# Optimization experiments

Hardware: AMD Instinct MI355X
Metric: run time of the kernel (lower is better)

Reference implementation:

```python
import jax, jax.numpy as jnp
import numpy as np

N_NODES = 100000
N_EDGES = 3200000
BATCH = 16
HIDDEN = 64


def setup_inputs() -> dict:
    key = jax.random.key(0)
    k_mu, k_ei, k_w1, k_b1, k_w2, k_b2 = jax.random.split(key, 6)
    mu = jax.random.normal(k_mu, (BATCH, N_NODES), dtype=jnp.float32)
    edge_index = jax.random.randint(k_ei, (2, N_EDGES), 0, N_NODES, dtype=jnp.int64)
    # MLP params: Linear(1, hidden) -> GELU -> Linear(hidden, 1)
    W1 = jax.random.normal(k_w1, (1, HIDDEN), dtype=jnp.float32) * (1.0 / np.sqrt(1))
    b1 = jax.random.normal(k_b1, (HIDDEN,), dtype=jnp.float32) * 0.02
    W2 = jax.random.normal(k_w2, (HIDDEN, 1), dtype=jnp.float32) * (1.0 / np.sqrt(HIDDEN))
    b2 = jax.random.normal(k_b2, (1,), dtype=jnp.float32) * 0.02
    return {"mu": mu, "edge_index": edge_index, "W1": W1, "b1": b1, "W2": W2, "b2": b2}


def reference(mu, edge_index, W1, b1, W2, b2):
    row, col = edge_index[0], edge_index[1]
    B, N = mu.shape
    # degree of each destination node (clamped at 1)
    deg = jax.ops.segment_sum(jnp.ones_like(row, dtype=mu.dtype), row, num_segments=N)
    deg = jnp.maximum(deg, 1.0)  # [N]
    # batched message aggregation: gather source values, scatter-add to rows
    msgs = mu[:, col].T                                    # [E, B]
    agg = jax.ops.segment_sum(msgs, row, num_segments=N)   # [N, B]
    out = agg.T / deg[None, :]                             # [B, N]
    # tiny MLP applied per scalar: 1 -> hidden -> 1 with exact (erf) GELU
    h = jax.nn.gelu(out[..., None] * W1[0][None, None, :] + b1, approximate=False)  # [B, N, H]
    y = jnp.einsum('bnh,h->bn', h, W2[:, 0]) + b2[0]       # [B, N]
    return y
```

## Files before the change

### kernel.cpp

```cpp
#include <hip/hip_runtime.h>
#include <hip/hip_fp16.h>

#define N_NODES 100000
#define N_EDGES 3200000
#define BATCH   16
#define HIDDEN  64

#define NBINS   512
#define NPB     196
#define NSH     8
#define CAP_SH  1024
#define CAP_BIN 8192
#define EPB     8192
#define MAXW    16

#define PBLKS   391
#define TBLKS   196
#define LBLKS   17

#define LUT_SIZE  8192
#define LUT_LO    (-16.0f)
#define LUT_SCALE (LUT_SIZE / 32.0f)

typedef int v4i __attribute__((ext_vector_type(4)));

__global__ __launch_bounds__(512) void fused_part_prep_kernel(
    const int* __restrict__ ei, unsigned int* __restrict__ gcnt,
    unsigned int* __restrict__ packed,
    const float* __restrict__ mu, __half* __restrict__ mu_h,
    const float* __restrict__ W1, const float* __restrict__ b1,
    const float* __restrict__ W2, const float* __restrict__ b2,
    float* __restrict__ lut) {
  __shared__ int aux[NBINS];
  __shared__ int dlt[NBINS];
  __shared__ int wsum[8];
  __shared__ unsigned int stag[EPB];
  __shared__ unsigned short sbin[EPB];

  int blk = blockIdx.x;
  int t = threadIdx.x;

  if (blk < TBLKS + LBLKS) {
    if (blk < TBLKS) {
      int n = blk * 512 + t;
      if (n >= N_NODES) return;
      float4 o[4];
#pragma unroll
      for (int q = 0; q < 4; ++q) {
        o[q].x = mu[(q * 4 + 0) * N_NODES + n];
        o[q].y = mu[(q * 4 + 1) * N_NODES + n];
        o[q].z = mu[(q * 4 + 2) * N_NODES + n];
        o[q].w = mu[(q * 4 + 3) * N_NODES + n];
      }
      __half2 hh[8];
#pragma unroll
      for (int q = 0; q < 4; ++q) {
        hh[2 * q]     = __floats2half2_rn(o[q].x, o[q].y);
        hh[2 * q + 1] = __floats2half2_rn(o[q].z, o[q].w);
      }
      int4 w0 = make_int4(*(int*)&hh[0], *(int*)&hh[1], *(int*)&hh[2], *(int*)&hh[3]);
      int4 w1 = make_int4(*(int*)&hh[4], *(int*)&hh[5], *(int*)&hh[6], *(int*)&hh[7]);
      int4* dst = (int4*)(mu_h + (size_t)n * BATCH);
      dst[0] = w0;
      dst[1] = w1;
    } else {
      int i = (blk - TBLKS) * 512 + t;
      if (i > LUT_SIZE) return;
      float x = LUT_LO + (float)i / LUT_SCALE;
      float acc = b2[0];
      for (int h = 0; h < HIDDEN; ++h) {
        float z = fmaf(x, W1[h], b1[h]);
        float g = 0.5f * z * (1.0f + erff(z * 0.70710678118654752f));
        acc = fmaf(g, W2[h], acc);
      }
      lut[i] = acc;
    }
    return;
  }

  int pblk = blk - (TBLKS + LBLKS);
  int base = pblk * EPB;
  int nvalid = min(EPB, N_EDGES - base);
  int sh = pblk & (NSH - 1);
  aux[t] = 0;
  __syncthreads();

  unsigned int pk[16];
  int bn[16];
  int rk[16];
  if (t * 16 + 16 <= nvalid) {
    const v4i* rp = (const v4i*)(ei + base + t * 16);
    const v4i* cp = (const v4i*)(ei + N_EDGES + base + t * 16);
    v4i rr[4], cc[4];
#pragma unroll
    for (int q = 0; q < 4; ++q) {
      rr[q] = rp[q];
      cc[q] = cp[q];
    }
#pragma unroll
    for (int q = 0; q < 4; ++q) {
#pragma unroll
      for (int u = 0; u < 4; ++u) {
        int k = q * 4 + u;
        int r = rr[q][u];
        int c = cc[q][u];
        int b = r / NPB;
        int rl = r - b * NPB;
        pk[k] = ((unsigned int)rl << 17) | (unsigned int)c;
        bn[k] = b;
      }
    }
#pragma unroll
    for (int k = 0; k < 16; ++k) rk[k] = atomicAdd(&aux[bn[k]], 1);
  } else {
#pragma unroll
    for (int k = 0; k < 16; ++k) {
      int e = t * 16 + k;
      if (e < nvalid) {
        int r = ei[base + e];
        int c = ei[N_EDGES + base + e];
        int b = r / NPB;
        int rl = r - b * NPB;
        pk[k] = ((unsigned int)rl << 17) | (unsigned int)c;
        bn[k] = b;
        rk[k] = atomicAdd(&aux[b], 1);
      } else {
        bn[k] = -1;
      }
    }
  }
  __syncthreads();

  int lane = t & 63;
  int wid = t >> 6;
  int v = aux[t];

  unsigned int gb = v ? atomicAdd(&gcnt[t * NSH + sh], (unsigned int)v) : 0u;

  int sv = v;
#pragma unroll
  for (int d = 1; d < 64; d <<= 1) {
    int n = __shfl_up(sv, d, 64);
    if (lane >= d) sv += n;
  }
  if (lane == 63) wsum[wid] = sv;
  __syncthreads();
  if (t < 8) {
    int s = wsum[t];
#pragma unroll
    for (int d = 1; d < 8; d <<= 1) {
      int n = __shfl_up(s, d, 8);
      if (t >= d) s += n;
    }
    wsum[t] = s;
  }
  __syncthreads();
  int pexcl = sv + (wid ? wsum[wid - 1] : 0) - v;
  aux[t] = pexcl;
  dlt[t] = (int)(sh * CAP_SH + gb) - pexcl;
  __syncthreads();

#pragma unroll
  for (int k = 0; k < 16; ++k) {
    if (bn[k] >= 0) {
      int p = aux[bn[k]] + rk[k];
      stag[p] = pk[k];
      sbin[p] = (unsigned short)bn[k];
    }
  }
  __syncthreads();

  unsigned int lim = (unsigned int)((sh + 1) * CAP_SH);
  for (int i = t; i < nvalid; i += 512) {
    int b = sbin[i];
    unsigned int pos = (unsigned int)(i + dlt[b]);
    if (pos < lim)
      packed[(size_t)b * CAP_BIN + pos] = stag[i];
  }
}

__global__ __launch_bounds__(512) void scatter_apply_kernel(
    const unsigned int* __restrict__ gcnt, const unsigned int* __restrict__ packed,
    const __half* __restrict__ mu_h, const float* __restrict__ lut,
    float* __restrict__ out) {
  __shared__ unsigned int scol[CAP_BIN];
  __shared__ int dcnt[NPB];
  __shared__ int ebase[NPB];
  __shared__ int wpart[4];
  __shared__ int scnt_s[NSH];

  int t = threadIdx.x;
  int bin = blockIdx.x;

  const unsigned int* pp = packed + (size_t)bin * CAP_BIN;

  if (t < NPB) dcnt[t] = 0;
  if (t < NSH) scnt_s[t] = min((int)gcnt[bin * NSH + t], CAP_SH);
  __syncthreads();

  unsigned int w[MAXW];
  {
    const uint4* pp4 = (const uint4*)pp;
#pragma unroll
    for (int q = 0; q < 4; ++q) {
      uint4 a = pp4[t * 4 + q];
      w[q * 4 + 0] = a.x;
      w[q * 4 + 1] = a.y;
      w[q * 4 + 2] = a.z;
      w[q * 4 + 3] = a.w;
    }
  }

  int rk[MAXW];
#pragma unroll
  for (int k = 0; k < MAXW; ++k) {
    int i = t * 16 + k;
    int off = i & (CAP_SH - 1);
    rk[k] = (off < scnt_s[i >> 10]) ? atomicAdd(&dcnt[w[k] >> 17], 1) : 0;
  }
  __syncthreads();

  int v = 0, sv = 0;
  if (t < 256) {
    v = (t < NPB) ? dcnt[t] : 0;
    int lane = t & 63;
    sv = v;
#pragma unroll
    for (int d = 1; d < 64; d <<= 1) {
      int n = __shfl_up(sv, d, 64);
      if (lane >= d) sv += n;
    }
    if (lane == 63) wpart[t >> 6] = sv;
  }
  __syncthreads();
  if (t < 256) {
    int wid = t >> 6;
    int off = 0;
#pragma unroll
    for (int q = 0; q < 3; ++q)
      if (wid > q) off += wpart[q];
    if (t < NPB) ebase[t] = sv + off - v;
  }
  __syncthreads();

#pragma unroll
  for (int k = 0; k < MAXW; ++k) {
    int i = t * 16 + k;
    int off = i & (CAP_SH - 1);
    if (off < scnt_s[i >> 10]) {
      int rl = (int)(w[k] >> 17);
      scol[ebase[rl] + rk[k]] = w[k] & 0x1FFFFu;
    }
  }
  __syncthreads();

  const __half2* mu2 = (const __half2*)mu_h;
  int j2 = t & 7;
  int nsl = t >> 3;
  int binBase = bin * NPB;

#pragma unroll
  for (int pass = 0; pass < 4; ++pass) {
    int nl = pass * 64 + nsl;
    if (nl < NPB) {
      int node = binBase + nl;
      if (node < N_NODES) {
        int s = ebase[nl];
        int e = s + dcnt[nl];
        float2 a0 = {0.f, 0.f}, a1 = {0.f, 0.f};
        float2 a2 = {0.f, 0.f}, a3 = {0.f, 0.f};
        int i = s;
        for (; i + 8 <= e; i += 8) {
          int c0 = (int)scol[i];
          int c1 = (int)scol[i + 1];
          int c2 = (int)scol[i + 2];
          int c3 = (int)scol[i + 3];
          int c4 = (int)scol[i + 4];
          int c5 = (int)scol[i + 5];
          int c6 = (int)scol[i + 6];
          int c7 = (int)scol[i + 7];
          __half2 v0 = mu2[(size_t)c0 * 8 + j2];
          __half2 v1 = mu2[(size_t)c1 * 8 + j2];
          __half2 v2 = mu2[(size_t)c2 * 8 + j2];
          __half2 v3 = mu2[(size_t)c3 * 8 + j2];
          __half2 v4 = mu2[(size_t)c4 * 8 + j2];
          __half2 v5 = mu2[(size_t)c5 * 8 + j2];
          __half2 v6 = mu2[(size_t)c6 * 8 + j2];
          __half2 v7 = mu2[(size_t)c7 * 8 + j2];
          float2 f0 = __half22float2(v0);
          float2 f1 = __half22float2(v1);
          float2 f2 = __half22float2(v2);
          float2 f3 = __half22float2(v3);
          float2 f4 = __half22float2(v4);
          float2 f5 = __half22float2(v5);
          float2 f6 = __half22float2(v6);
          float2 f7 = __half22float2(v7);
          a0.x += f0.x + f4.x; a0.y += f0.y + f4.y;
          a1.x += f1.x + f5.x; a1.y += f1.y + f5.y;
          a2.x += f2.x + f6.x; a2.y += f2.y + f6.y;
          a3.x += f3.x + f7.x; a3.y += f3.y + f7.y;
        }
        for (; i + 4 <= e; i += 4) {
          int c0 = (int)scol[i];
          int c1 = (int)scol[i + 1];
          int c2 = (int)scol[i + 2];
          int c3 = (int)scol[i + 3];
          __half2 v0 = mu2[(size_t)c0 * 8 + j2];
          __half2 v1 = mu2[(size_t)c1 * 8 + j2];
          __half2 v2 = mu2[(size_t)c2 * 8 + j2];
          __half2 v3 = mu2[(size_t)c3 * 8 + j2];
          float2 f0 = __half22float2(v0);
          float2 f1 = __half22float2(v1);
          float2 f2 = __half22float2(v2);
          float2 f3 = __half22float2(v3);
          a0.x += f0.x; a0.y += f0.y;
          a1.x += f1.x; a1.y += f1.y;
          a2.x += f2.x; a2.y += f2.y;
          a3.x += f3.x; a3.y += f3.y;
        }
        for (; i < e; ++i) {
          float2 f = __half22float2(mu2[(size_t)scol[i] * 8 + j2]);
          a0.x += f.x; a0.y += f.y;
        }
        float sx = (a0.x + a1.x) + (a2.x + a3.x);
        float sy = (a0.y + a1.y) + (a2.y + a3.y);
        float dinv = 1.0f / (float)max(e - s, 1);

        float xs[2] = {sx * dinv, sy * dinv};
#pragma unroll
        for (int q = 0; q < 2; ++q) {
          float u = (xs[q] - LUT_LO) * LUT_SCALE;
          u = fminf(fmaxf(u, 0.0f), (float)LUT_SIZE - 0.001f);
          int ii = (int)u;
          float frac = u - (float)ii;
          float lo = lut[ii];
          float hi = lut[ii + 1];
          __builtin_nontemporal_store(fmaf(hi - lo, frac, lo),
                                      &out[(size_t)(2 * j2 + q) * N_NODES + node]);
        }
      }
    }
  }
}

extern "C" void kernel_launch(void* const* d_in, const int* in_sizes, int n_in,
                              void* d_out, int out_size, void* d_ws, size_t ws_size,
                              hipStream_t stream) {
  const float* mu = (const float*)d_in[0];
  const int*   ei = (const int*)d_in[1];
  const float* W1 = (const float*)d_in[2];
  const float* b1 = (const float*)d_in[3];
  const float* W2 = (const float*)d_in[4];
  const float* b2 = (const float*)d_in[5];
  float* out = (float*)d_out;

  __half* mu_h = (__half*)d_ws;
  float* lut  = (float*)(mu_h + (size_t)N_NODES * BATCH);
  unsigned int* gcnt = (unsigned int*)(lut + LUT_SIZE + 1);
  unsigned int* packed = gcnt + NBINS * NSH;

  (void)hipMemsetAsync(gcnt, 0, NBINS * NSH * sizeof(unsigned int), stream);

  fused_part_prep_kernel<<<PBLKS + TBLKS + LBLKS, 512, 0, stream>>>(
      ei, gcnt, packed, mu, mu_h, W1, b1, W2, b2, lut);

  scatter_apply_kernel<<<NBINS, 512, 0, stream>>>(gcnt, packed, mu_h, lut, out);
}
```

Baseline: 124.4 us.

## Fold transpose and LUT work into partition blocks; stage LUT in shared memory

The half-precision transpose of mu and the GELU-MLP lookup-table build no longer run in their own blocks. Each of the 391 partition blocks now does a slice of both before its bucketing work, so the launch shrinks to the partition grid. The scatter/apply kernel copies the whole 8193-entry LUT into shared memory per block and interpolates from there, and its output stores become ordinary stores instead of nontemporal ones. Both kernels get a min-blocks launch-bounds hint. The trade-off is that every scatter block pays a 32 KB LUT copy and carries more LDS, which can lower occupancy. The partition blocks also have to wait at the barrier for the serial 64-step erf loop.

```diff
diff --git a/kernel.cpp b/kernel.cpp
--- a/kernel.cpp
+++ b/kernel.cpp
@@ -15,8 +15,8 @@
 #define MAXW    16
 
 #define PBLKS   391
-#define TBLKS   196
-#define LBLKS   17
+#define NPT     256
+#define LPT     21
 
 #define LUT_SIZE  8192
 #define LUT_LO    (-16.0f)
@@ -24,7 +24,7 @@
 
 typedef int v4i __attribute__((ext_vector_type(4)));
 
-__global__ __launch_bounds__(512) void fused_part_prep_kernel(
+__global__ __launch_bounds__(512, 4) void fused_part_prep_kernel(
     const int* __restrict__ ei, unsigned int* __restrict__ gcnt,
     unsigned int* __restrict__ packed,
     const float* __restrict__ mu, __half* __restrict__ mu_h,
@@ -37,13 +37,14 @@
   __shared__ unsigned int stag[EPB];
   __shared__ unsigned short sbin[EPB];
 
-  int blk = blockIdx.x;
+  int pblk = blockIdx.x;
   int t = threadIdx.x;
 
-  if (blk < TBLKS + LBLKS) {
-    if (blk < TBLKS) {
-      int n = blk * 512 + t;
-      if (n >= N_NODES) return;
+  aux[t] = 0;
+
+  if (t < NPT) {
+    int n = pblk * NPT + t;
+    if (n < N_NODES) {
       float4 o[4];
 #pragma unroll
       for (int q = 0; q < 4; ++q) {
@@ -63,9 +64,10 @@
       int4* dst = (int4*)(mu_h + (size_t)n * BATCH);
       dst[0] = w0;
       dst[1] = w1;
-    } else {
-      int i = (blk - TBLKS) * 512 + t;
-      if (i > LUT_SIZE) return;
+    }
+  } else if (t < NPT + LPT) {
+    int i = pblk * LPT + (t - NPT);
+    if (i <= LUT_SIZE) {
       float x = LUT_LO + (float)i / LUT_SCALE;
       float acc = b2[0];
       for (int h = 0; h < HIDDEN; ++h) {
@@ -75,15 +77,12 @@
       }
       lut[i] = acc;
     }
-    return;
-  }
-
-  int pblk = blk - (TBLKS + LBLKS);
+  }
+  __syncthreads();
+
   int base = pblk * EPB;
   int nvalid = min(EPB, N_EDGES - base);
   int sh = pblk & (NSH - 1);
-  aux[t] = 0;
-  __syncthreads();
 
   unsigned int pk[16];
   int bn[16];
@@ -179,11 +178,12 @@
   }
 }
 
-__global__ __launch_bounds__(512) void scatter_apply_kernel(
+__global__ __launch_bounds__(512, 4) void scatter_apply_kernel(
     const unsigned int* __restrict__ gcnt, const unsigned int* __restrict__ packed,
     const __half* __restrict__ mu_h, const float* __restrict__ lut,
     float* __restrict__ out) {
   __shared__ unsigned int scol[CAP_BIN];
+  __shared__ float lut_s[LUT_SIZE + 1];
   __shared__ int dcnt[NPB];
   __shared__ int ebase[NPB];
   __shared__ int wpart[4];
@@ -196,6 +196,14 @@
 
   if (t < NPB) dcnt[t] = 0;
   if (t < NSH) scnt_s[t] = min((int)gcnt[bin * NSH + t], CAP_SH);
+
+  {
+    const float4* l4 = (const float4*)lut;
+    float4* s4 = (float4*)lut_s;
+#pragma unroll
+    for (int j = 0; j < 4; ++j) s4[t + j * 512] = l4[t + j * 512];
+    if (t == 0) lut_s[LUT_SIZE] = lut[LUT_SIZE];
+  }
   __syncthreads();
 
   unsigned int w[MAXW];
@@ -333,10 +341,9 @@
           u = fminf(fmaxf(u, 0.0f), (float)LUT_SIZE - 0.001f);
           int ii = (int)u;
           float frac = u - (float)ii;
-          float lo = lut[ii];
-          float hi = lut[ii + 1];
-          __builtin_nontemporal_store(fmaf(hi - lo, frac, lo),
-                                      &out[(size_t)(2 * j2 + q) * N_NODES + node]);
+          float lo = lut_s[ii];
+          float hi = lut_s[ii + 1];
+          out[(size_t)(2 * j2 + q) * N_NODES + node] = fmaf(hi - lo, frac, lo);
         }
       }
     }
@@ -361,7 +368,7 @@
 
   (void)hipMemsetAsync(gcnt, 0, NBINS * NSH * sizeof(unsigned int), stream);
 
-  fused_part_prep_kernel<<<PBLKS + TBLKS + LBLKS, 512, 0, stream>>>(
+  fused_part_prep_kernel<<<PBLKS, 512, 0, stream>>>(
       ei, gcnt, packed, mu, mu_h, W1, b1, W2, b2, lut);
 
   scatter_apply_kernel<<<NBINS, 512, 0, stream>>>(gcnt, packed, mu_h, lut, out);
```

After: 133.0 us. 6.9% more time.

## Replace per-node CSR sort with LDS float atomic accumulation in scatter kernel

Applied to the files above, without the earlier changes.

The scatter kernel no longer builds a per-node CSR inside each bin (atomic rank, prefix scan, reorder). Instead it compacts the edge words into LDS, counts degrees, and then walks edges in order, gathering half-precision mu values and accumulating them into a padded shared-memory accumulator with float atomics. The output stage then reads the accumulator per (batch, node) with coalesced stores. This removes two barriers and the scan, at the cost of many LDS float atomics with possible contention and a non-deterministic summation order.

```diff
diff --git a/kernel.cpp b/kernel.cpp
--- a/kernel.cpp
+++ b/kernel.cpp
@@ -12,7 +12,7 @@
 #define CAP_SH  1024
 #define CAP_BIN 8192
 #define EPB     8192
-#define MAXW    16
+#define ACCW    17
 
 #define PBLKS   391
 #define TBLKS   196
@@ -184,161 +184,77 @@
     const __half* __restrict__ mu_h, const float* __restrict__ lut,
     float* __restrict__ out) {
   __shared__ unsigned int scol[CAP_BIN];
+  __shared__ float acc[NPB * ACCW];
   __shared__ int dcnt[NPB];
-  __shared__ int ebase[NPB];
-  __shared__ int wpart[4];
   __shared__ int scnt_s[NSH];
 
   int t = threadIdx.x;
   int bin = blockIdx.x;
-
   const unsigned int* pp = packed + (size_t)bin * CAP_BIN;
 
+  for (int i = t; i < NPB * ACCW; i += 512) acc[i] = 0.0f;
   if (t < NPB) dcnt[t] = 0;
   if (t < NSH) scnt_s[t] = min((int)gcnt[bin * NSH + t], CAP_SH);
   __syncthreads();
 
-  unsigned int w[MAXW];
+  int pfx[NSH + 1];
+  pfx[0] = 0;
+#pragma unroll
+  for (int q = 0; q < NSH; ++q) pfx[q + 1] = pfx[q] + scnt_s[q];
+  int cnt = pfx[NSH];
+
   {
     const uint4* pp4 = (const uint4*)pp;
+    uint4 a[4];
+#pragma unroll
+    for (int q = 0; q < 4; ++q) a[q] = pp4[t * 4 + q];
 #pragma unroll
     for (int q = 0; q < 4; ++q) {
-      uint4 a = pp4[t * 4 + q];
-      w[q * 4 + 0] = a.x;
-      w[q * 4 + 1] = a.y;
-      w[q * 4 + 2] = a.z;
-      w[q * 4 + 3] = a.w;
-    }
-  }
-
-  int rk[MAXW];
-#pragma unroll
-  for (int k = 0; k < MAXW; ++k) {
-    int i = t * 16 + k;
-    int off = i & (CAP_SH - 1);
-    rk[k] = (off < scnt_s[i >> 10]) ? atomicAdd(&dcnt[w[k] >> 17], 1) : 0;
-  }
-  __syncthreads();
-
-  int v = 0, sv = 0;
-  if (t < 256) {
-    v = (t < NPB) ? dcnt[t] : 0;
-    int lane = t & 63;
-    sv = v;
-#pragma unroll
-    for (int d = 1; d < 64; d <<= 1) {
-      int n = __shfl_up(sv, d, 64);
-      if (lane >= d) sv += n;
-    }
-    if (lane == 63) wpart[t >> 6] = sv;
-  }
-  __syncthreads();
-  if (t < 256) {
-    int wid = t >> 6;
-    int off = 0;
-#pragma unroll
-    for (int q = 0; q < 3; ++q)
-      if (wid > q) off += wpart[q];
-    if (t < NPB) ebase[t] = sv + off - v;
-  }
-  __syncthreads();
-
-#pragma unroll
-  for (int k = 0; k < MAXW; ++k) {
-    int i = t * 16 + k;
-    int off = i & (CAP_SH - 1);
-    if (off < scnt_s[i >> 10]) {
-      int rl = (int)(w[k] >> 17);
-      scol[ebase[rl] + rk[k]] = w[k] & 0x1FFFFu;
-    }
-  }
-  __syncthreads();
-
+      unsigned int wq[4] = {a[q].x, a[q].y, a[q].z, a[q].w};
+#pragma unroll
+      for (int u = 0; u < 4; ++u) {
+        int i = t * 16 + q * 4 + u;
+        int sh = i >> 10;
+        int off = i & (CAP_SH - 1);
+        if (off < scnt_s[sh]) {
+          unsigned int wv = wq[u];
+          scol[pfx[sh] + off] = wv;
+          atomicAdd(&dcnt[wv >> 17], 1);
+        }
+      }
+    }
+  }
+  __syncthreads();
+
+  int j2 = t & 7;
+  int es0 = t >> 3;
   const __half2* mu2 = (const __half2*)mu_h;
-  int j2 = t & 7;
-  int nsl = t >> 3;
+  for (int i = es0; i < cnt; i += 64) {
+    unsigned int wv = scol[i];
+    int rl = (int)(wv >> 17);
+    int c  = (int)(wv & 0x1FFFFu);
+    float2 f = __half22float2(mu2[(size_t)c * 8 + j2]);
+    atomicAdd(&acc[rl * ACCW + 2 * j2],     f.x);
+    atomicAdd(&acc[rl * ACCW + 2 * j2 + 1], f.y);
+  }
+  __syncthreads();
+
   int binBase = bin * NPB;
-
-#pragma unroll
-  for (int pass = 0; pass < 4; ++pass) {
-    int nl = pass * 64 + nsl;
-    if (nl < NPB) {
-      int node = binBase + nl;
-      if (node < N_NODES) {
-        int s = ebase[nl];
-        int e = s + dcnt[nl];
-        float2 a0 = {0.f, 0.f}, a1 = {0.f, 0.f};
-        float2 a2 = {0.f, 0.f}, a3 = {0.f, 0.f};
-        int i = s;
-        for (; i + 8 <= e; i += 8) {
-          int c0 = (int)scol[i];
-          int c1 = (int)scol[i + 1];
-          int c2 = (int)scol[i + 2];
-          int c3 = (int)scol[i + 3];
-          int c4 = (int)scol[i + 4];
-          int c5 = (int)scol[i + 5];
-          int c6 = (int)scol[i + 6];
-          int c7 = (int)scol[i + 7];
-          __half2 v0 = mu2[(size_t)c0 * 8 + j2];
-          __half2 v1 = mu2[(size_t)c1 * 8 + j2];
-          __half2 v2 = mu2[(size_t)c2 * 8 + j2];
-          __half2 v3 = mu2[(size_t)c3 * 8 + j2];
-          __half2 v4 = mu2[(size_t)c4 * 8 + j2];
-          __half2 v5 = mu2[(size_t)c5 * 8 + j2];
-          __half2 v6 = mu2[(size_t)c6 * 8 + j2];
-          __half2 v7 = mu2[(size_t)c7 * 8 + j2];
-          float2 f0 = __half22float2(v0);
-          float2 f1 = __half22float2(v1);
-          float2 f2 = __half22float2(v2);
-          float2 f3 = __half22float2(v3);
-          float2 f4 = __half22float2(v4);
-          float2 f5 = __half22float2(v5);
-          float2 f6 = __half22float2(v6);
-          float2 f7 = __half22float2(v7);
-          a0.x += f0.x + f4.x; a0.y += f0.y + f4.y;
-          a1.x += f1.x + f5.x; a1.y += f1.y + f5.y;
-          a2.x += f2.x + f6.x; a2.y += f2.y + f6.y;
-          a3.x += f3.x + f7.x; a3.y += f3.y + f7.y;
-        }
-        for (; i + 4 <= e; i += 4) {
-          int c0 = (int)scol[i];
-          int c1 = (int)scol[i + 1];
-          int c2 = (int)scol[i + 2];
-          int c3 = (int)scol[i + 3];
-          __half2 v0 = mu2[(size_t)c0 * 8 + j2];
-          __half2 v1 = mu2[(size_t)c1 * 8 + j2];
-          __half2 v2 = mu2[(size_t)c2 * 8 + j2];
-          __half2 v3 = mu2[(size_t)c3 * 8 + j2];
-          float2 f0 = __half22float2(v0);
-          float2 f1 = __half22float2(v1);
-          float2 f2 = __half22float2(v2);
-          float2 f3 = __half22float2(v3);
-          a0.x += f0.x; a0.y += f0.y;
-          a1.x += f1.x; a1.y += f1.y;
-          a2.x += f2.x; a2.y += f2.y;
-          a3.x += f3.x; a3.y += f3.y;
-        }
-        for (; i < e; ++i) {
-          float2 f = __half22float2(mu2[(size_t)scol[i] * 8 + j2]);
-          a0.x += f.x; a0.y += f.y;
-        }
-        float sx = (a0.x + a1.x) + (a2.x + a3.x);
-        float sy = (a0.y + a1.y) + (a2.y + a3.y);
-        float dinv = 1.0f / (float)max(e - s, 1);
-
-        float xs[2] = {sx * dinv, sy * dinv};
-#pragma unroll
-        for (int q = 0; q < 2; ++q) {
-          float u = (xs[q] - LUT_LO) * LUT_SCALE;
-          u = fminf(fmaxf(u, 0.0f), (float)LUT_SIZE - 0.001f);
-          int ii = (int)u;
-          float frac = u - (float)ii;
-          float lo = lut[ii];
-          float hi = lut[ii + 1];
-          __builtin_nontemporal_store(fmaf(hi - lo, frac, lo),
-                                      &out[(size_t)(2 * j2 + q) * N_NODES + node]);
-        }
-      }
+  for (int idx = t; idx < BATCH * NPB; idx += 512) {
+    int j = idx / NPB;
+    int nl = idx - j * NPB;
+    int node = binBase + nl;
+    if (node < N_NODES) {
+      float dinv = 1.0f / (float)max(dcnt[nl], 1);
+      float x = acc[nl * ACCW + j] * dinv;
+      float u = (x - LUT_LO) * LUT_SCALE;
+      u = fminf(fmaxf(u, 0.0f), (float)LUT_SIZE - 0.001f);
+      int ii = (int)u;
+      float frac = u - (float)ii;
+      float lo = lut[ii];
+      float hi = lut[ii + 1];
+      __builtin_nontemporal_store(fmaf(hi - lo, frac, lo),
+                                  &out[(size_t)j * N_NODES + node]);
     }
   }
 }
```

Result: slower. 367.9 us (+195.7%).
